# Kernel tuning notes

Measured on AMD Instinct MI355X. Metric: run time of the kernel, lower is better.

## Reference

```python
import jax, jax.numpy as jnp
import numpy as np

B, S, D, H = 2, 2048, 1024, 16
DK = D // H


def setup_inputs() -> dict:
    key = jax.random.key(0)
    ks = jax.random.split(key, 11)
    scale = 1.0 / np.sqrt(D)
    inp = {
        "q": jax.random.normal(ks[0], (B, S, D), jnp.float32),
        "k": jax.random.normal(ks[1], (B, S, D), jnp.float32),
        "v": jax.random.normal(ks[2], (B, S, D), jnp.float32),
        # causal mask, broadcastable to (B, H, S, S); 0 = masked
        "mask": jnp.tril(jnp.ones((S, S), jnp.int32))[None, None, :, :],
        "wq": jax.random.normal(ks[3], (D, D), jnp.float32) * scale,
        "bq": jax.random.normal(ks[4], (D,), jnp.float32) * scale,
        "wk": jax.random.normal(ks[5], (D, D), jnp.float32) * scale,
        "bk": jax.random.normal(ks[6], (D,), jnp.float32) * scale,
        "wv": jax.random.normal(ks[7], (D, D), jnp.float32) * scale,
        "bv": jax.random.normal(ks[8], (D,), jnp.float32) * scale,
        "wo": jax.random.normal(ks[9], (D, D), jnp.float32) * scale,
        "bo": jax.random.normal(ks[10], (D,), jnp.float32) * scale,
    }
    return inp


def reference(q, k, v, mask, wq, bq, wk, bk, wv, bv, wo, bo):
    # Linear projections (torch Linear: y = x @ W^T + b)
    Q = jnp.einsum('bsd,ed->bse', q, wq) + bq
    K = jnp.einsum('bsd,ed->bse', k, wk) + bk
    V = jnp.einsum('bsd,ed->bse', v, wv) + bv
    # split heads -> (B, H, S, d_k)
    Q = Q.reshape(B, S, H, DK).transpose(0, 2, 1, 3)
    K = K.reshape(B, S, H, DK).transpose(0, 2, 1, 3)
    V = V.reshape(B, S, H, DK).transpose(0, 2, 1, 3)
    # naive full-score attention, faithful to the source
    scores = jnp.einsum('bhqd,bhkd->bhqk', Q, K) / jnp.sqrt(jnp.float32(DK))
    scores = jnp.where(mask == 0, -jnp.inf, scores)
    attn = jax.nn.softmax(scores, axis=-1)
    out = jnp.einsum('bhqk,bhkd->bhqd', attn, V)
    # merge heads -> (B, S, D)
    out = out.transpose(0, 2, 1, 3).reshape(B, S, D)
    return jnp.einsum('bsd,ed->bse', out, wo) + bo
```

## Files before the change

kernel.cpp:

```cpp
#include <hip/hip_runtime.h>
#include <hip/hip_bf16.h>
#include <cstdint>

constexpr int Bc = 2, Sc = 2048, Dc = 1024, Hc = 16;
constexpr int Mtok = Bc * Sc;
constexpr float SCL = 0.125f * 1.44269504089f;

typedef __bf16 bf16;
typedef __bf16 bf16x4 __attribute__((ext_vector_type(4)));
typedef __bf16 bf16x8 __attribute__((ext_vector_type(8)));
typedef float  f32x4  __attribute__((ext_vector_type(4)));
typedef float  f32x16 __attribute__((ext_vector_type(16)));
typedef unsigned u32x4 __attribute__((ext_vector_type(4)));

__device__ __forceinline__ void gld_lds16(const bf16* g, bf16* l) {
  __builtin_amdgcn_global_load_lds(
      (__attribute__((address_space(1))) void*)(void*)g,
      (__attribute__((address_space(3))) void*)l, 16, 0, 0);
}

__device__ __forceinline__ bf16x8 ld8u(const bf16* p) {
  bf16x4 lo = *(const bf16x4*)p;
  bf16x4 hi = *(const bf16x4*)(p + 4);
  return __builtin_shufflevector(lo, hi, 0, 1, 2, 3, 4, 5, 6, 7);
}
__device__ __forceinline__ void st8u(bf16* p, bf16x8 v) {
  *(bf16x4*)p       = __builtin_shufflevector(v, v, 0, 1, 2, 3);
  *(bf16x4*)(p + 4) = __builtin_shufflevector(v, v, 4, 5, 6, 7);
}

__global__ __launch_bounds__(256) void convert_all(
    const float* __restrict__ q, const float* __restrict__ k,
    const float* __restrict__ v, const float* __restrict__ wq,
    const float* __restrict__ wk, const float* __restrict__ wv,
    const float* __restrict__ wo, bf16* __restrict__ ws)
{
  constexpr size_t NQ = (size_t)Mtok * Dc;
  constexpr size_t NW = (size_t)Dc * Dc;
  const size_t e = ((size_t)blockIdx.x * 256 + threadIdx.x) * 8;
  const float* src; bf16* dst;
  float scl = 1.0f;
  if (e < 3 * NQ) {
    src = (e < NQ) ? q + e : (e < 2 * NQ) ? k + (e - NQ) : v + (e - 2 * NQ);
    dst = ws + e;
  } else {
    const size_t w = e - 3 * NQ;
    const float* wsrc = (w < NW) ? wq : (w < 2 * NW) ? wk : (w < 3 * NW) ? wv : wo;
    if (w < NW) scl = SCL;
    src = wsrc + (w & (NW - 1));
    dst = ws + 5 * NQ + w;
  }
  f32x4 a = ((const f32x4*)src)[0];
  f32x4 b = ((const f32x4*)src)[1];
  bf16x8 t;
  t[0]=(bf16)(a[0]*scl); t[1]=(bf16)(a[1]*scl); t[2]=(bf16)(a[2]*scl); t[3]=(bf16)(a[3]*scl);
  t[4]=(bf16)(b[0]*scl); t[5]=(bf16)(b[1]*scl); t[6]=(bf16)(b[2]*scl); t[7]=(bf16)(b[3]*scl);
  *(bf16x8*)dst = t;
}

__global__ __launch_bounds__(256, 6) void gemm_qkv(
    const bf16* __restrict__ Aq, const bf16* __restrict__ Ak,
    const bf16* __restrict__ Av, const bf16* __restrict__ Wb,
    const float* __restrict__ bq, const float* __restrict__ bk,
    const float* __restrict__ bv,
    bf16* __restrict__ Yq, bf16* __restrict__ Yk, bf16* __restrict__ Vt)
{
  __shared__ __attribute__((aligned(16))) bf16 As[64 * 64];
  __shared__ __attribute__((aligned(16))) bf16 Bs[128 * 64];

  const int z = blockIdx.z;
  const bf16*  A    = (z == 0) ? Aq : (z == 1) ? Ak : Av;
  const bf16*  Wz   = Wb + (size_t)z * Dc * Dc;
  const float* bias = (z == 0) ? bq : (z == 1) ? bk : bv;

  const int m0 = blockIdx.x * 64, n0 = blockIdx.y * 128;
  const int tid = threadIdx.x, wave = tid >> 6, lane = tid & 63;
  const int quad = lane >> 4, l16 = lane & 15;
  const int swz = l16 & 7;
  const int sr  = lane >> 3;
  const int scol = ((lane & 7) ^ sr) * 8;

  f32x4 acc[4][2] = {};

  for (int k0 = 0; k0 < Dc; k0 += 64) {
#pragma unroll
    for (int j = 0; j < 2; ++j)
      gld_lds16(A + (size_t)(m0 + wave * 16 + j * 8 + sr) * Dc + k0 + scol,
                &As[(wave * 16 + j * 8) * 64]);
#pragma unroll
    for (int j = 0; j < 4; ++j)
      gld_lds16(Wz + (size_t)(n0 + wave * 32 + j * 8 + sr) * Dc + k0 + scol,
                &Bs[(wave * 32 + j * 8) * 64]);
    __syncthreads();
#pragma unroll
    for (int ks = 0; ks < 2; ++ks) {
      const int pc = ((ks * 4 + quad) ^ swz) * 8;
      bf16x8 af[4];
#pragma unroll
      for (int rt = 0; rt < 4; ++rt)
        af[rt] = *(const bf16x8*)&As[(rt * 16 + l16) * 64 + pc];
#pragma unroll
      for (int ct = 0; ct < 2; ++ct) {
        bf16x8 bfr = *(const bf16x8*)&Bs[(wave * 32 + ct * 16 + l16) * 64 + pc];
#pragma unroll
        for (int rt = 0; rt < 4; ++rt)
          acc[rt][ct] = __builtin_amdgcn_mfma_f32_16x16x32_bf16(af[rt], bfr, acc[rt][ct], 0, 0, 0);
      }
    }
    __syncthreads();
  }

  if (z < 2) {
    bf16* Y = (z == 0) ? Yq : Yk;
    const float bscl = (z == 0) ? SCL : 1.0f;
#pragma unroll
    for (int ct = 0; ct < 2; ++ct) {
      const int col = n0 + wave * 32 + ct * 16 + l16;
      const float bvv = bias[col] * bscl;
#pragma unroll
      for (int rt = 0; rt < 4; ++rt)
#pragma unroll
        for (int i = 0; i < 4; ++i) {
          const int row = m0 + rt * 16 + quad * 4 + i;
          Y[(size_t)row * Dc + col] = (bf16)(acc[rt][ct][i] + bvv);
        }
    }
  } else {
#pragma unroll
    for (int ct = 0; ct < 2; ++ct) {
      const int col = n0 + wave * 32 + ct * 16 + l16;
      const float bvv = bias[col];
#pragma unroll
      for (int rt = 0; rt < 4; ++rt) {
        const int row0 = m0 + rt * 16 + quad * 4;
        const int bb = row0 >> 11, s0 = row0 & 2047;
        bf16x4 pk;
#pragma unroll
        for (int i = 0; i < 4; ++i) pk[i] = (bf16)(acc[rt][ct][i] + bvv);
        *(bf16x4*)&Vt[((size_t)bb * Dc + col) * Sc + s0] = pk;
      }
    }
  }
}

__global__ __launch_bounds__(256, 4) void gemm_o(
    const bf16* __restrict__ A, const bf16* __restrict__ Wz,
    const float* __restrict__ bias, float* __restrict__ Y)
{
  __shared__ __attribute__((aligned(16))) bf16 As[64 * 64];
  __shared__ __attribute__((aligned(16))) bf16 Bs[64 * 64];

  const int m0 = blockIdx.x * 64, n0 = blockIdx.y * 64;
  const int tid = threadIdx.x, wave = tid >> 6, lane = tid & 63;
  const int quad = lane >> 4, l16 = lane & 15;
  const int swz = l16 & 7;
  const int sr  = lane >> 3;
  const int scol = ((lane & 7) ^ sr) * 8;

  f32x4 acc[4] = {};

  for (int k0 = 0; k0 < Dc; k0 += 64) {
#pragma unroll
    for (int j = 0; j < 2; ++j) {
      gld_lds16(A  + (size_t)(m0 + wave * 16 + j * 8 + sr) * Dc + k0 + scol,
                &As[(wave * 16 + j * 8) * 64]);
      gld_lds16(Wz + (size_t)(n0 + wave * 16 + j * 8 + sr) * Dc + k0 + scol,
                &Bs[(wave * 16 + j * 8) * 64]);
    }
    __syncthreads();
#pragma unroll
    for (int ks = 0; ks < 2; ++ks) {
      const int pc = ((ks * 4 + quad) ^ swz) * 8;
      bf16x8 bfr = *(const bf16x8*)&Bs[(wave * 16 + l16) * 64 + pc];
#pragma unroll
      for (int rt = 0; rt < 4; ++rt) {
        bf16x8 af = *(const bf16x8*)&As[(rt * 16 + l16) * 64 + pc];
        acc[rt] = __builtin_amdgcn_mfma_f32_16x16x32_bf16(af, bfr, acc[rt], 0, 0, 0);
      }
    }
    __syncthreads();
  }

  const int col = n0 + wave * 16 + l16;
  const float bvv = bias[col];
#pragma unroll
  for (int rt = 0; rt < 4; ++rt)
#pragma unroll
    for (int i = 0; i < 4; ++i) {
      const int row = m0 + rt * 16 + quad * 4 + i;
      Y[(size_t)row * Dc + col] = acc[rt][i] + bvv;
    }
}

template <bool AF32, bool BF32, bool OUTF32>
__global__ __launch_bounds__(256) void gemm128(
    const void* __restrict__ Av, const void* __restrict__ Bv,
    const float* __restrict__ bias, void* __restrict__ Yv,
    int M, int N, int K)
{
  __shared__ __attribute__((aligned(16))) bf16 As[2][128][40];
  __shared__ __attribute__((aligned(16))) bf16 Bs[2][128][40];

  const int m0 = blockIdx.x * 128, n0 = blockIdx.y * 128;
  const int tid = threadIdx.x, wave = tid >> 6, lane = tid & 63;
  const int quad = lane >> 4, l16 = lane & 15;
  const int rw = wave >> 1, cw = wave & 1;
  const int srow = tid >> 1, sc = (tid & 1) * 16;

  f32x4 acc[4][4] = {};

  auto load = [&](const void* P, bool f32, int r0, int k0, bf16x8& lo, bf16x8& hi) {
    if (f32) {
      const float* s = (const float*)P + (size_t)(r0 + srow) * K + k0 + sc;
      f32x4 a0 = ((const f32x4*)s)[0], a1 = ((const f32x4*)s)[1];
      f32x4 a2 = ((const f32x4*)s)[2], a3 = ((const f32x4*)s)[3];
      lo[0]=(bf16)a0[0]; lo[1]=(bf16)a0[1]; lo[2]=(bf16)a0[2]; lo[3]=(bf16)a0[3];
      lo[4]=(bf16)a1[0]; lo[5]=(bf16)a1[1]; lo[6]=(bf16)a1[2]; lo[7]=(bf16)a1[3];
      hi[0]=(bf16)a2[0]; hi[1]=(bf16)a2[1]; hi[2]=(bf16)a2[2]; hi[3]=(bf16)a2[3];
      hi[4]=(bf16)a3[0]; hi[5]=(bf16)a3[1]; hi[6]=(bf16)a3[2]; hi[7]=(bf16)a3[3];
    } else {
      const bf16* s = (const bf16*)P + (size_t)(r0 + srow) * K + k0 + sc;
      lo = ((const bf16x8*)s)[0]; hi = ((const bf16x8*)s)[1];
    }
  };

  bf16x8 alo, ahi, blo, bhi;
  load(Av, AF32, m0, 0, alo, ahi); load(Bv, BF32, n0, 0, blo, bhi);
  *(bf16x8*)&As[0][srow][sc] = alo; *(bf16x8*)&As[0][srow][sc + 8] = ahi;
  *(bf16x8*)&Bs[0][srow][sc] = blo; *(bf16x8*)&Bs[0][srow][sc + 8] = bhi;

  const int NIT = K >> 5;
  for (int it = 0; it < NIT; ++it) {
    __syncthreads();
    const int cur = it & 1;
    const bool pf = (it + 1) < NIT;
    if (pf) { load(Av, AF32, m0, (it+1)*32, alo, ahi); load(Bv, BF32, n0, (it+1)*32, blo, bhi); }

    bf16x8 af[4];
#pragma unroll
    for (int rt = 0; rt < 4; ++rt)
      af[rt] = *(const bf16x8*)&As[cur][rw * 64 + rt * 16 + l16][quad * 8];
#pragma unroll
    for (int ct = 0; ct < 4; ++ct) {
      bf16x8 bfr = *(const bf16x8*)&Bs[cur][cw * 64 + ct * 16 + l16][quad * 8];
#pragma unroll
      for (int rt = 0; rt < 4; ++rt)
        acc[rt][ct] = __builtin_amdgcn_mfma_f32_16x16x32_bf16(af[rt], bfr, acc[rt][ct], 0, 0, 0);
    }
    if (pf) {
      const int nxt = cur ^ 1;
      *(bf16x8*)&As[nxt][srow][sc] = alo; *(bf16x8*)&As[nxt][srow][sc + 8] = ahi;
      *(bf16x8*)&Bs[nxt][srow][sc] = blo; *(bf16x8*)&Bs[nxt][srow][sc + 8] = bhi;
    }
  }

#pragma unroll
  for (int ct = 0; ct < 4; ++ct) {
    const int col = n0 + cw * 64 + ct * 16 + l16;
    const float bvv = bias[col];
#pragma unroll
    for (int rt = 0; rt < 4; ++rt)
#pragma unroll
      for (int i = 0; i < 4; ++i) {
        const int row = m0 + rw * 64 + rt * 16 + quad * 4 + i;
        const float vv = acc[rt][ct][i] + bvv;
        if constexpr (OUTF32) ((float*)Yv)[(size_t)row * N + col] = vv;
        else                  ((bf16*)Yv)[(size_t)row * N + col] = (bf16)vv;
      }
  }
}

__global__ __launch_bounds__(256) void transpose_v(
    const bf16* __restrict__ in, bf16* __restrict__ out)
{
  __shared__ __attribute__((aligned(16))) bf16 tile[64][72];
  const int s0 = blockIdx.x * 64, d0 = blockIdx.y * 64, b = blockIdx.z;
  const int t = threadIdx.x, r = t >> 2, c = (t & 3) * 16;

  const bf16* src = in + (size_t)(b * Sc + s0 + r) * Dc + d0 + c;
  *(bf16x8*)&tile[r][c]     = ((const bf16x8*)src)[0];
  *(bf16x8*)&tile[r][c + 8] = ((const bf16x8*)src)[1];
  __syncthreads();

  bf16x8 t0, t1;
#pragma unroll
  for (int j = 0; j < 8; ++j) t0[j] = tile[c + j][r];
#pragma unroll
  for (int j = 0; j < 8; ++j) t1[j] = tile[c + 8 + j][r];
  bf16* dst = out + (size_t)(b * Dc + d0 + r) * Sc + s0 + c;
  ((bf16x8*)dst)[0] = t0;
  ((bf16x8*)dst)[1] = t1;
}

template <bool PRE>
__global__ __launch_bounds__(256, 4) void attn11(
    const bf16* __restrict__ Q, const bf16* __restrict__ K,
    const bf16* __restrict__ Vt, bf16* __restrict__ O)
{
  union SMem {
    struct { bf16 Ks[2][64][68]; bf16 Vs[2][64][68]; } m;
    struct { float Ob[2][32][64]; float lb[2][32]; } x;
  };
  __shared__ __attribute__((aligned(16))) SMem sm;
  __shared__ float ls[2][32];

  const int bh = blockIdx.x, b = bh >> 4, h = bh & 15;
  const int yy = blockIdx.y;
  const int qt = (yy < 16) ? (31 - yy) : (yy - 16);
  const int q0 = qt * 64;
  const int nK = qt + 1;
  const int c  = (nK + 1) >> 1;

  const int tid = threadIdx.x, wave = tid >> 6, lane = tid & 63;
  const int w = wave & 1, g = wave >> 1;
  const int l32 = lane & 31, hi = lane >> 5;
  const int hi4 = hi * 4, hi8 = hi * 8;
  const int qg = q0 + w * 32 + l32;

  const int sg = tid >> 7, lt = tid & 127;
  const int row2 = lt >> 1, c32 = (lt & 1) * 32;
  const bf16* Kb = K  + ((size_t)(b * Sc + row2)) * Dc + h * 64 + c32;
  const bf16* Vb = Vt + ((size_t)(b * Dc + h * 64 + row2)) * Sc + c32;

  const bf16* qp = Q + (size_t)(b * Sc + qg) * Dc + h * 64;
  bf16x8 qf0 = *(const bf16x8*)(qp + 0 * 16 + hi8);
  bf16x8 qf1 = *(const bf16x8*)(qp + 1 * 16 + hi8);
  bf16x8 qf2 = *(const bf16x8*)(qp + 2 * 16 + hi8);
  bf16x8 qf3 = *(const bf16x8*)(qp + 3 * 16 + hi8);

  f32x16 oacc0 = {}, oacc1 = {};
  float lsum = 0.f;
  bf16x8 kr0, kr1, kr2, kr3, vr0, vr1, vr2, vr3;

  auto LOADS = [&](int kb) {
    const bf16* kp = Kb + (size_t)kb * 64 * Dc;
    kr0 = *(const bf16x8*)kp;        kr1 = *(const bf16x8*)(kp + 8);
    kr2 = *(const bf16x8*)(kp + 16); kr3 = *(const bf16x8*)(kp + 24);
    const bf16* vp = Vb + kb * 64;
    vr0 = *(const bf16x8*)vp;        vr1 = *(const bf16x8*)(vp + 8);
    vr2 = *(const bf16x8*)(vp + 16); vr3 = *(const bf16x8*)(vp + 24);
  };
  auto WRITES = [&]() {
    st8u(&sm.m.Ks[sg][row2][c32],      kr0); st8u(&sm.m.Ks[sg][row2][c32 + 8],  kr1);
    st8u(&sm.m.Ks[sg][row2][c32 + 16], kr2); st8u(&sm.m.Ks[sg][row2][c32 + 24], kr3);
    st8u(&sm.m.Vs[sg][row2][c32],      vr0); st8u(&sm.m.Vs[sg][row2][c32 + 8],  vr1);
    st8u(&sm.m.Vs[sg][row2][c32 + 16], vr2); st8u(&sm.m.Vs[sg][row2][c32 + 24], vr3);
  };

#define MHA_PK(R0, R1, DST)                                                   \
  do {                                                                        \
    float p0 = PRE ? __builtin_amdgcn_exp2f(s[R0])                            \
                   : __builtin_amdgcn_exp2f(s[R0] * SCL);                     \
    float p1 = PRE ? __builtin_amdgcn_exp2f(s[R1])                            \
                   : __builtin_amdgcn_exp2f(s[R1] * SCL);                     \
    if (dg) {                                                                 \
      p0 = ((((R0) & 3) + (((R0) >> 2) << 3) + hi4) <= kq) ? p0 : 0.f;        \
      p1 = ((((R1) & 3) + (((R1) >> 2) << 3) + hi4) <= kq) ? p1 : 0.f;        \
    }                                                                         \
    lp += p0 + p1;                                                            \
    const bf16 b0 = (bf16)p0, b1 = (bf16)p1;                                  \
    DST = (unsigned)__builtin_bit_cast(unsigned short, b0) |                  \
          ((unsigned)__builtin_bit_cast(unsigned short, b1) << 16);           \
  } while (0)

  auto TILE = [&](int kb, bool dg) {
    const int kqb = qg - kb * 64;
#pragma unroll
    for (int blk = 0; blk < 2; ++blk) {
      if (dg && w == 0 && blk == 1) continue;
      f32x16 s = {};
      __builtin_amdgcn_s_setprio(1);
      {
        bf16x8 ak = ld8u(&sm.m.Ks[g][blk * 32 + l32][0 * 16 + hi8]);
        s = __builtin_amdgcn_mfma_f32_32x32x16_bf16(ak, qf0, s, 0, 0, 0);
        ak = ld8u(&sm.m.Ks[g][blk * 32 + l32][1 * 16 + hi8]);
        s = __builtin_amdgcn_mfma_f32_32x32x16_bf16(ak, qf1, s, 0, 0, 0);
        ak = ld8u(&sm.m.Ks[g][blk * 32 + l32][2 * 16 + hi8]);
        s = __builtin_amdgcn_mfma_f32_32x32x16_bf16(ak, qf2, s, 0, 0, 0);
        ak = ld8u(&sm.m.Ks[g][blk * 32 + l32][3 * 16 + hi8]);
        s = __builtin_amdgcn_mfma_f32_32x32x16_bf16(ak, qf3, s, 0, 0, 0);
      }
      __builtin_amdgcn_s_setprio(0);
      const int kq = kqb - blk * 32;
      float lp = 0.f;
      unsigned w0, w1, w2, w3, w4r, w5, w6, w7;
      MHA_PK(0, 1, w0);   MHA_PK(2, 3, w1);
      MHA_PK(4, 5, w2);   MHA_PK(6, 7, w3);
      MHA_PK(8, 9, w4r);  MHA_PK(10, 11, w5);
      MHA_PK(12, 13, w6); MHA_PK(14, 15, w7);
      lsum += lp;
      asm volatile("v_permlane32_swap_b32 %0, %1" : "+v"(w0), "+v"(w2));
      asm volatile("v_permlane32_swap_b32 %0, %1" : "+v"(w1), "+v"(w3));
      asm volatile("v_permlane32_swap_b32 %0, %1" : "+v"(w4r), "+v"(w6));
      asm volatile("v_permlane32_swap_b32 %0, %1" : "+v"(w5), "+v"(w7));
      const u32x4 ua = {w0, w1, w2, w3};
      const u32x4 ub = {w4r, w5, w6, w7};
      const bf16x8 f0 = __builtin_bit_cast(bf16x8, ua);
      const bf16x8 f1 = __builtin_bit_cast(bf16x8, ub);
      __builtin_amdgcn_s_setprio(1);
      {
        const int kc0 = (blk * 2 + 0) * 16 + hi8;
        const int kc1 = (blk * 2 + 1) * 16 + hi8;
        bf16x8 bv = ld8u(&sm.m.Vs[g][0 * 32 + l32][kc0]);
        oacc0 = __builtin_amdgcn_mfma_f32_32x32x16_bf16(f0, bv, oacc0, 0, 0, 0);
        bv = ld8u(&sm.m.Vs[g][1 * 32 + l32][kc0]);
        oacc1 = __builtin_amdgcn_mfma_f32_32x32x16_bf16(f0, bv, oacc1, 0, 0, 0);
        bv = ld8u(&sm.m.Vs[g][0 * 32 + l32][kc1]);
        oacc0 = __builtin_amdgcn_mfma_f32_32x32x16_bf16(f1, bv, oacc0, 0, 0, 0);
        bv = ld8u(&sm.m.Vs[g][1 * 32 + l32][kc1]);
        oacc1 = __builtin_amdgcn_mfma_f32_32x32x16_bf16(f1, bv, oacc1, 0, 0, 0);
      }
      __builtin_amdgcn_s_setprio(0);
    }
  };
#undef MHA_PK

  if (sg ? (c < nK) : true) { LOADS(sg ? c : 0); WRITES(); }
  asm volatile("s_waitcnt lgkmcnt(0)" ::: "memory");
  __builtin_amdgcn_s_barrier();

  for (int i = 0; i < c; ++i) {
    const bool pfv = sg ? (c + i + 1 < nK) : (i + 1 < c);
    if (pfv) LOADS(sg ? (c + i + 1) : (i + 1));
    const int kb = g ? (c + i) : i;
    if (kb < nK) TILE(kb, kb == qt);
    __builtin_amdgcn_s_barrier();
    if (pfv) WRITES();
    asm volatile("s_waitcnt lgkmcnt(0)" ::: "memory");
    __builtin_amdgcn_s_barrier();
  }

  float la = lsum, lb2 = lsum;
  asm volatile("v_permlane32_swap_b32 %0, %1" : "+v"(la), "+v"(lb2));
  const float ltot = la + lb2;

  asm volatile("" ::: "memory");
  if (g == 1) {
#pragma unroll
    for (int r = 0; r < 16; ++r) {
      const int qr = (r & 3) + ((r >> 2) << 3) + hi4;
      sm.x.Ob[w][qr][l32]      = oacc0[r];
      sm.x.Ob[w][qr][32 + l32] = oacc1[r];
    }
    if (hi == 0) sm.x.lb[w][l32] = ltot;
  }
  asm volatile("s_waitcnt lgkmcnt(0)" ::: "memory");
  __builtin_amdgcn_s_barrier();
  asm volatile("" ::: "memory");
  if (g == 0) {
    const float rlt = 1.0f / (ltot + sm.x.lb[w][l32]);
    if (hi == 0) ls[w][l32] = rlt;
    asm volatile("s_waitcnt lgkmcnt(0)" ::: "memory");
#pragma unroll
    for (int r = 0; r < 16; ++r) {
      const int qr = (r & 3) + ((r >> 2) << 3) + hi4;
      const float rl = ls[w][qr];
      const size_t orow = (size_t)(b * Sc + q0 + w * 32 + qr) * Dc + h * 64;
      O[orow + l32]      = (bf16)((oacc0[r] + sm.x.Ob[w][qr][l32]) * rl);
      O[orow + 32 + l32] = (bf16)((oacc1[r] + sm.x.Ob[w][qr][32 + l32]) * rl);
    }
  }
}

extern "C" void kernel_launch(void* const* d_in, const int* in_sizes, int n_in,
                              void* d_out, int out_size, void* d_ws, size_t ws_size,
                              hipStream_t stream)
{
  const float* q  = (const float*)d_in[0];
  const float* k  = (const float*)d_in[1];
  const float* v  = (const float*)d_in[2];
  const float* wq = (const float*)d_in[4];
  const float* bq = (const float*)d_in[5];
  const float* wk = (const float*)d_in[6];
  const float* bk = (const float*)d_in[7];
  const float* wv = (const float*)d_in[8];
  const float* bv = (const float*)d_in[9];
  const float* wo = (const float*)d_in[10];
  const float* bo = (const float*)d_in[11];
  float* out = (float*)d_out;

  constexpr size_t NQ = (size_t)Mtok * Dc;
  constexpr size_t NW = (size_t)Dc * Dc;
  bf16* W = (bf16*)d_ws;
  const dim3 ga(Hc * Bc, 32);
  const dim3 gt(Sc / 64, Dc / 64, Bc);

  const bool fancy = ws_size >= (size_t)(6 * NQ + 4 * NW) * 2;
  if (fancy) {
    bf16* xq = W;
    bf16* xk = W + NQ;
    bf16* xv = W + 2 * NQ;
    bf16* Qp = W + 3 * NQ;
    bf16* Kp = W + 4 * NQ;
    bf16* wb = W + 5 * NQ;
    bf16* Vt = W + 5 * NQ + 4 * NW;
    bf16* AO = W;

    convert_all<<<8192, 256, 0, stream>>>(q, k, v, wq, wk, wv, wo, W);
    gemm_qkv<<<dim3(Mtok / 64, Dc / 128, 3), 256, 0, stream>>>(
        xq, xk, xv, wb, bq, bk, bv, Qp, Kp, Vt);
    attn11<true><<<ga, 256, 0, stream>>>(Qp, Kp, Vt, AO);
    gemm_o<<<dim3(Mtok / 64, Dc / 64), 256, 0, stream>>>(AO, wb + 3 * NW, bo, out);
  } else {
    bf16* Qp = W;
    bf16* Kp = W + NQ;
    bf16* Vp = W + 2 * NQ;
    bf16* Vt = W + 3 * NQ;
    bf16* AO = W + 4 * NQ;
    const dim3 gg(Mtok / 128, Dc / 128);
    gemm128<true, true, false><<<gg, 256, 0, stream>>>(q, wq, bq, Qp, Mtok, Dc, Dc);
    gemm128<true, true, false><<<gg, 256, 0, stream>>>(k, wk, bk, Kp, Mtok, Dc, Dc);
    gemm128<true, true, false><<<gg, 256, 0, stream>>>(v, wv, bv, Vp, Mtok, Dc, Dc);
    transpose_v<<<gt, 256, 0, stream>>>(Vp, Vt);
    attn11<false><<<ga, 256, 0, stream>>>(Qp, Kp, Vt, AO);
    gemm128<false, true, true><<<gg, 256, 0, stream>>>(AO, wo, bo, out, Mtok, Dc, Dc);
  }
}
```

Measured before the change: 223.8 us.

## Load V operands directly from global into registers instead of staging through LDS

The attention kernel stops staging V tiles in shared memory. Each wave now loads its V MFMA operands straight from the transposed V in global memory at the start of each key tile, and the P·V MFMAs take them from registers. This removes the LDS writes and reads for V and halves the shared-memory footprint. In exchange, V global-load latency lands on the critical path without double buffering, V data is re-read per wave (likely served from cache), and launch bounds drop from 4 to 3 blocks per CU to give room for the extra registers.

```diff
diff --git a/kernel.cpp b/kernel.cpp
--- a/kernel.cpp
+++ b/kernel.cpp
@@ -293,12 +293,12 @@
 }
 
 template <bool PRE>
-__global__ __launch_bounds__(256, 4) void attn11(
+__global__ __launch_bounds__(256, 3) void attn12(
     const bf16* __restrict__ Q, const bf16* __restrict__ K,
     const bf16* __restrict__ Vt, bf16* __restrict__ O)
 {
   union SMem {
-    struct { bf16 Ks[2][64][68]; bf16 Vs[2][64][68]; } m;
+    struct { bf16 Ks[2][64][68]; } m;
     struct { float Ob[2][32][64]; float lb[2][32]; } x;
   };
   __shared__ __attribute__((aligned(16))) SMem sm;
@@ -319,8 +319,10 @@
 
   const int sg = tid >> 7, lt = tid & 127;
   const int row2 = lt >> 1, c32 = (lt & 1) * 32;
-  const bf16* Kb = K  + ((size_t)(b * Sc + row2)) * Dc + h * 64 + c32;
-  const bf16* Vb = Vt + ((size_t)(b * Dc + h * 64 + row2)) * Sc + c32;
+  const bf16* Kb = K + ((size_t)(b * Sc + row2)) * Dc + h * 64 + c32;
+
+  const bf16* vpd0 = Vt + ((size_t)(b * Dc + h * 64 + l32)) * Sc;
+  const bf16* vpd1 = vpd0 + (size_t)32 * Sc;
 
   const bf16* qp = Q + (size_t)(b * Sc + qg) * Dc + h * 64;
   bf16x8 qf0 = *(const bf16x8*)(qp + 0 * 16 + hi8);
@@ -330,21 +332,16 @@
 
   f32x16 oacc0 = {}, oacc1 = {};
   float lsum = 0.f;
-  bf16x8 kr0, kr1, kr2, kr3, vr0, vr1, vr2, vr3;
+  bf16x8 kr0, kr1, kr2, kr3;
 
   auto LOADS = [&](int kb) {
     const bf16* kp = Kb + (size_t)kb * 64 * Dc;
     kr0 = *(const bf16x8*)kp;        kr1 = *(const bf16x8*)(kp + 8);
     kr2 = *(const bf16x8*)(kp + 16); kr3 = *(const bf16x8*)(kp + 24);
-    const bf16* vp = Vb + kb * 64;
-    vr0 = *(const bf16x8*)vp;        vr1 = *(const bf16x8*)(vp + 8);
-    vr2 = *(const bf16x8*)(vp + 16); vr3 = *(const bf16x8*)(vp + 24);
   };
   auto WRITES = [&]() {
     st8u(&sm.m.Ks[sg][row2][c32],      kr0); st8u(&sm.m.Ks[sg][row2][c32 + 8],  kr1);
     st8u(&sm.m.Ks[sg][row2][c32 + 16], kr2); st8u(&sm.m.Ks[sg][row2][c32 + 24], kr3);
-    st8u(&sm.m.Vs[sg][row2][c32],      vr0); st8u(&sm.m.Vs[sg][row2][c32 + 8],  vr1);
-    st8u(&sm.m.Vs[sg][row2][c32 + 16], vr2); st8u(&sm.m.Vs[sg][row2][c32 + 24], vr3);
   };
 
 #define MHA_PK(R0, R1, DST)                                                   \
@@ -363,57 +360,63 @@
           ((unsigned)__builtin_bit_cast(unsigned short, b1) << 16);           \
   } while (0)
 
-  auto TILE = [&](int kb, bool dg) {
-    const int kqb = qg - kb * 64;
-#pragma unroll
-    for (int blk = 0; blk < 2; ++blk) {
-      if (dg && w == 0 && blk == 1) continue;
-      f32x16 s = {};
-      __builtin_amdgcn_s_setprio(1);
-      {
-        bf16x8 ak = ld8u(&sm.m.Ks[g][blk * 32 + l32][0 * 16 + hi8]);
-        s = __builtin_amdgcn_mfma_f32_32x32x16_bf16(ak, qf0, s, 0, 0, 0);
-        ak = ld8u(&sm.m.Ks[g][blk * 32 + l32][1 * 16 + hi8]);
-        s = __builtin_amdgcn_mfma_f32_32x32x16_bf16(ak, qf1, s, 0, 0, 0);
-        ak = ld8u(&sm.m.Ks[g][blk * 32 + l32][2 * 16 + hi8]);
-        s = __builtin_amdgcn_mfma_f32_32x32x16_bf16(ak, qf2, s, 0, 0, 0);
-        ak = ld8u(&sm.m.Ks[g][blk * 32 + l32][3 * 16 + hi8]);
-        s = __builtin_amdgcn_mfma_f32_32x32x16_bf16(ak, qf3, s, 0, 0, 0);
-      }
-      __builtin_amdgcn_s_setprio(0);
-      const int kq = kqb - blk * 32;
-      float lp = 0.f;
-      unsigned w0, w1, w2, w3, w4r, w5, w6, w7;
-      MHA_PK(0, 1, w0);   MHA_PK(2, 3, w1);
-      MHA_PK(4, 5, w2);   MHA_PK(6, 7, w3);
-      MHA_PK(8, 9, w4r);  MHA_PK(10, 11, w5);
-      MHA_PK(12, 13, w6); MHA_PK(14, 15, w7);
-      lsum += lp;
-      asm volatile("v_permlane32_swap_b32 %0, %1" : "+v"(w0), "+v"(w2));
-      asm volatile("v_permlane32_swap_b32 %0, %1" : "+v"(w1), "+v"(w3));
-      asm volatile("v_permlane32_swap_b32 %0, %1" : "+v"(w4r), "+v"(w6));
-      asm volatile("v_permlane32_swap_b32 %0, %1" : "+v"(w5), "+v"(w7));
-      const u32x4 ua = {w0, w1, w2, w3};
-      const u32x4 ub = {w4r, w5, w6, w7};
-      const bf16x8 f0 = __builtin_bit_cast(bf16x8, ua);
-      const bf16x8 f1 = __builtin_bit_cast(bf16x8, ub);
-      __builtin_amdgcn_s_setprio(1);
-      {
-        const int kc0 = (blk * 2 + 0) * 16 + hi8;
-        const int kc1 = (blk * 2 + 1) * 16 + hi8;
-        bf16x8 bv = ld8u(&sm.m.Vs[g][0 * 32 + l32][kc0]);
-        oacc0 = __builtin_amdgcn_mfma_f32_32x32x16_bf16(f0, bv, oacc0, 0, 0, 0);
-        bv = ld8u(&sm.m.Vs[g][1 * 32 + l32][kc0]);
-        oacc1 = __builtin_amdgcn_mfma_f32_32x32x16_bf16(f0, bv, oacc1, 0, 0, 0);
-        bv = ld8u(&sm.m.Vs[g][0 * 32 + l32][kc1]);
-        oacc0 = __builtin_amdgcn_mfma_f32_32x32x16_bf16(f1, bv, oacc0, 0, 0, 0);
-        bv = ld8u(&sm.m.Vs[g][1 * 32 + l32][kc1]);
-        oacc1 = __builtin_amdgcn_mfma_f32_32x32x16_bf16(f1, bv, oacc1, 0, 0, 0);
-      }
-      __builtin_amdgcn_s_setprio(0);
-    }
+  auto SUB = [&](int krow, int kq, bool dg,
+                 bf16x8 v00, bf16x8 v10, bf16x8 v01, bf16x8 v11) {
+    f32x16 s = {};
+    __builtin_amdgcn_s_setprio(1);
+    {
+      bf16x8 ak = ld8u(&sm.m.Ks[g][krow + l32][0 * 16 + hi8]);
+      s = __builtin_amdgcn_mfma_f32_32x32x16_bf16(ak, qf0, s, 0, 0, 0);
+      ak = ld8u(&sm.m.Ks[g][krow + l32][1 * 16 + hi8]);
+      s = __builtin_amdgcn_mfma_f32_32x32x16_bf16(ak, qf1, s, 0, 0, 0);
+      ak = ld8u(&sm.m.Ks[g][krow + l32][2 * 16 + hi8]);
+      s = __builtin_amdgcn_mfma_f32_32x32x16_bf16(ak, qf2, s, 0, 0, 0);
+      ak = ld8u(&sm.m.Ks[g][krow + l32][3 * 16 + hi8]);
+      s = __builtin_amdgcn_mfma_f32_32x32x16_bf16(ak, qf3, s, 0, 0, 0);
+    }
+    __builtin_amdgcn_s_setprio(0);
+    float lp = 0.f;
+    unsigned w0, w1, w2, w3, w4r, w5, w6, w7;
+    MHA_PK(0, 1, w0);   MHA_PK(2, 3, w1);
+    MHA_PK(4, 5, w2);   MHA_PK(6, 7, w3);
+    MHA_PK(8, 9, w4r);  MHA_PK(10, 11, w5);
+    MHA_PK(12, 13, w6); MHA_PK(14, 15, w7);
+    lsum += lp;
+    asm volatile("v_permlane32_swap_b32 %0, %1" : "+v"(w0), "+v"(w2));
+    asm volatile("v_permlane32_swap_b32 %0, %1" : "+v"(w1), "+v"(w3));
+    asm volatile("v_permlane32_swap_b32 %0, %1" : "+v"(w4r), "+v"(w6));
+    asm volatile("v_permlane32_swap_b32 %0, %1" : "+v"(w5), "+v"(w7));
+    const u32x4 ua = {w0, w1, w2, w3};
+    const u32x4 ub = {w4r, w5, w6, w7};
+    const bf16x8 f0 = __builtin_bit_cast(bf16x8, ua);
+    const bf16x8 f1 = __builtin_bit_cast(bf16x8, ub);
+    __builtin_amdgcn_s_setprio(1);
+    oacc0 = __builtin_amdgcn_mfma_f32_32x32x16_bf16(f0, v00, oacc0, 0, 0, 0);
+    oacc1 = __builtin_amdgcn_mfma_f32_32x32x16_bf16(f0, v10, oacc1, 0, 0, 0);
+    oacc0 = __builtin_amdgcn_mfma_f32_32x32x16_bf16(f1, v01, oacc0, 0, 0, 0);
+    oacc1 = __builtin_amdgcn_mfma_f32_32x32x16_bf16(f1, v11, oacc1, 0, 0, 0);
+    __builtin_amdgcn_s_setprio(0);
   };
 #undef MHA_PK
+
+  auto TILE = [&](int kb, bool dgt) {
+    const int kqb = qg - kb * 64;
+    const int co = kb * 64 + hi8;
+    bf16x8 va00 = *(const bf16x8*)(vpd0 + co);
+    bf16x8 va10 = *(const bf16x8*)(vpd1 + co);
+    bf16x8 va01 = *(const bf16x8*)(vpd0 + co + 16);
+    bf16x8 va11 = *(const bf16x8*)(vpd1 + co + 16);
+    const bool doB = !(dgt && w == 0);
+    bf16x8 vb00 = {}, vb10 = {}, vb01 = {}, vb11 = {};
+    if (doB) {
+      vb00 = *(const bf16x8*)(vpd0 + co + 32);
+      vb10 = *(const bf16x8*)(vpd1 + co + 32);
+      vb01 = *(const bf16x8*)(vpd0 + co + 48);
+      vb11 = *(const bf16x8*)(vpd1 + co + 48);
+    }
+    SUB(0, kqb, dgt, va00, va10, va01, va11);
+    if (doB) SUB(32, kqb - 32, dgt, vb00, vb10, vb01, vb11);
+  };
 
   if (sg ? (c < nK) : true) { LOADS(sg ? c : 0); WRITES(); }
   asm volatile("s_waitcnt lgkmcnt(0)" ::: "memory");
@@ -499,7 +502,7 @@
     convert_all<<<8192, 256, 0, stream>>>(q, k, v, wq, wk, wv, wo, W);
     gemm_qkv<<<dim3(Mtok / 64, Dc / 128, 3), 256, 0, stream>>>(
         xq, xk, xv, wb, bq, bk, bv, Qp, Kp, Vt);
-    attn11<true><<<ga, 256, 0, stream>>>(Qp, Kp, Vt, AO);
+    attn12<true><<<ga, 256, 0, stream>>>(Qp, Kp, Vt, AO);
     gemm_o<<<dim3(Mtok / 64, Dc / 64), 256, 0, stream>>>(AO, wb + 3 * NW, bo, out);
   } else {
     bf16* Qp = W;
@@ -512,7 +515,7 @@
     gemm128<true, true, false><<<gg, 256, 0, stream>>>(k, wk, bk, Kp, Mtok, Dc, Dc);
     gemm128<true, true, false><<<gg, 256, 0, stream>>>(v, wv, bv, Vp, Mtok, Dc, Dc);
     transpose_v<<<gt, 256, 0, stream>>>(Vp, Vt);
-    attn11<false><<<ga, 256, 0, stream>>>(Qp, Kp, Vt, AO);
+    attn12<false><<<ga, 256, 0, stream>>>(Qp, Kp, Vt, AO);
     gemm128<false, true, true><<<gg, 256, 0, stream>>>(AO, wo, bo, out, Mtok, Dc, Dc);
   }
 }
```

New measurement: 232.7 us. 3.9% more time.
